# Performance work log

Hardware: AMD Instinct MI355X
Metric: run time of the kernel (lower is better)

The kernel has to match this reference:

```python
import jax, jax.numpy as jnp
from jax import lax
import numpy as np

B, GRID, H = 128, 28, 64      # batch, 28x28 pixel grid, hidden size
NDIR = 4                      # feature_sz = number of scan directions
FC_HD, OUT = 512, 10


def setup_inputs() -> dict:
    key = jax.random.key(0)
    ks = jax.random.split(key, 8)
    s_u = 1.0 / np.sqrt(2 * H)
    inp = {
        "x":  jax.random.normal(ks[0], (B, GRID, GRID), dtype=jnp.float32),
        # per-direction MDLSTM gate params: 5 gates (i, f_left, f_up, o, g)
        "Wx": jax.random.normal(ks[1], (NDIR, 5 * H), dtype=jnp.float32) * 0.1,
        "U":  jax.random.normal(ks[2], (NDIR, 2 * H, 5 * H), dtype=jnp.float32) * s_u,
        "b":  jnp.zeros((NDIR, 5 * H), dtype=jnp.float32),
        # fc head
        "W1": jax.random.normal(ks[3], (NDIR * H, FC_HD), dtype=jnp.float32) / np.sqrt(NDIR * H),
        "b1": jnp.zeros((FC_HD,), dtype=jnp.float32),
        "W2": jax.random.normal(ks[4], (FC_HD, OUT), dtype=jnp.float32) / np.sqrt(FC_HD),
        "b2": jnp.zeros((OUT,), dtype=jnp.float32),
    }
    return inp


def _mdlstm_dir(xg, Wx, U, b):
    # xg: [GRID(rows), GRID(cols), B] scalar pixel per cell
    zeros = jnp.zeros((xg.shape[-1], H), dtype=xg.dtype)

    def col_step(carry, inp):
        h_left, c_left = carry
        x_pix, h_up, c_up = inp                     # [B], [B,H], [B,H]
        z = x_pix[:, None] * Wx + jnp.concatenate([h_left, h_up], -1) @ U + b
        i, f1, f2, o, g = jnp.split(z, 5, axis=-1)  # each [B,H]
        c = (jax.nn.sigmoid(i) * jnp.tanh(g)
             + jax.nn.sigmoid(f1) * c_left
             + jax.nn.sigmoid(f2) * c_up)
        h = jax.nn.sigmoid(o) * jnp.tanh(c)
        return (h, c), (h, c)

    def row_step(carry, x_row):
        h_up_row, c_up_row = carry                  # [GRID,B,H] previous row
        _, (h_row, c_row) = lax.scan(col_step, (zeros, zeros),
                                     (x_row, h_up_row, c_up_row))
        return (h_row, c_row), None

    init = (jnp.zeros((GRID,) + zeros.shape, xg.dtype),
            jnp.zeros((GRID,) + zeros.shape, xg.dtype))
    (h_last_row, _), _ = lax.scan(row_step, init, xg)
    return h_last_row[-1]                           # final (bottom-right) hidden [B,H]


def _forward(x, Wx, U, b, W1, b1, W2, b2):
    x2 = x.reshape(-1, GRID, GRID)
    # 4 scan directions via flips; scan always proceeds top-left -> bottom-right
    dirs = jnp.stack([x2,
                      x2[:, :, ::-1],
                      x2[:, ::-1, :],
                      x2[:, ::-1, ::-1]], 0)        # [4,B,GRID,GRID]
    dirs = jnp.transpose(dirs, (0, 2, 3, 1))        # [4,GRID,GRID,B]
    h = jax.vmap(_mdlstm_dir)(dirs, Wx, U, b)       # [4,B,H]
    h = jnp.transpose(h, (1, 0, 2)).reshape(-1, NDIR * H)
    z = jax.nn.relu(h @ W1 + b1)
    return jax.nn.softmax(z @ W2 + b2, axis=-1)


def reference(x, Wx, U, b, W1, b1, W2, b2):
    return _forward(x, Wx, U, b, W1, b1, W2, b2)
```

## Files before the change

kernel.cpp:

```cpp
#include <hip/hip_runtime.h>
#include <hip/hip_bf16.h>


#define GRIDN 28
#define BATCH 128
#define HID   64
#define NDIR  4
#define FC_HD 512
#define OUT_N 10
#define BT    2
#define NTHR  512
#define NSLOT 29
#define S_H   104
#define S_C   68

typedef _Float16 f16;
typedef _Float16 f16x8 __attribute__((ext_vector_type(8)));
typedef float    f32x4 __attribute__((ext_vector_type(4)));

#define LOG2E  1.44269504088896340736f
#define LOG2E2 2.88539008177792681472f

__device__ __forceinline__ float rcpf(float x) { return __builtin_amdgcn_rcpf(x); }
__device__ __forceinline__ float ex2(float x)  { return __builtin_amdgcn_exp2f(x); }

__global__ __launch_bounds__(NTHR)
void mdlstm_kernel(const float* __restrict__ x,
                   const float* __restrict__ Wx,
                   const float* __restrict__ U,
                   const float* __restrict__ bias,
                   float* __restrict__ Hout)
{
    const int d    = blockIdx.x & 3;
    const int tile = blockIdx.x >> 2;
    const int tid  = threadIdx.x;
    const int lane = tid & 63;
    const int wave = tid >> 6;
    const int wm   = wave >> 2;
    const int wh   = wave & 3;
    const int l16  = lane & 15;
    const int q    = lane >> 4;
    const int nb   = wh * 16 + l16;

    __shared__ __align__(16) f16 Fh[2][BT][NSLOT * S_H];
    __shared__ float             Fc[2][BT][NSLOT * S_C];
    __shared__ float             xs[GRIDN][GRIDN][BT];

    for (int i = tid; i < 2 * BT * NSLOT * S_H; i += NTHR) ((f16*)Fh)[i] = (f16)0.0f;
    for (int i = tid; i < 2 * BT * NSLOT * S_C; i += NTHR) ((float*)Fc)[i] = 0.0f;
    for (int i = tid; i < GRIDN * GRIDN * BT; i += NTHR) {
        int bl = i & 1, rc = i >> 1, c = rc % GRIDN, r = rc / GRIDN;
        int rr = (d & 2) ? (GRIDN - 1 - r) : r;
        int cc = (d & 1) ? (GRIDN - 1 - c) : c;
        xs[r][c][bl] = x[((tile * BT + bl) * GRIDN + rr) * GRIDN + cc];
    }

    f16x8 bf[5][5];
#pragma unroll
    for (int g = 0; g < 5; ++g) {
        const float sc = (g == 4) ? LOG2E2 : -LOG2E;
        int n = g * 64 + nb;
#pragma unroll
        for (int ks = 0; ks < 4; ++ks) {
            f16x8 v;
            int kb = ks * 32 + q * 8;
#pragma unroll
            for (int j = 0; j < 8; ++j)
                v[j] = (f16)(sc * U[(d * 128 + kb + j) * 320 + n]);
            bf[g][ks] = v;
        }
        f16x8 v5 = {(f16)0, (f16)0, (f16)0, (f16)0, (f16)0, (f16)0, (f16)0, (f16)0};
        if (q == 0) {
            v5[0] = (f16)(sc * Wx[d * 320 + n]);
            v5[1] = (f16)(sc * bias[d * 320 + n]);
        }
        bf[g][4] = v5;
    }
    __syncthreads();

    if (tid < 2 * BT * NSLOT) {
        int buf = tid / (BT * NSLOT), rem = tid % (BT * NSLOT);
        int b = rem / NSLOT, sl = rem % NSLOT;
        Fh[buf][b][sl * S_H + 65] = (f16)1.0f;
    }
    if (tid < BT) Fh[0][tid][27 * S_H + 64] = (f16)xs[0][0][tid];
    __syncthreads();

    auto step = [&](int t, int br) __attribute__((always_inline)) {
        const int bw  = br ^ 1;
        const int rlo = (t > GRIDN - 1) ? (t - (GRIDN - 1)) : 0;
        const int rhi = (t < GRIDN - 1) ? t : (GRIDN - 1);
        const int k   = rhi - rlo + 1;
        const int nM  = (2 * k + 15) >> 4;

        if (t < 2 * GRIDN - 2 && tid >= NTHR - 56) {
            int idx = tid - (NTHR - 56), b = idx & 1, j = idx >> 1;
            int rlo2 = (t + 1 > GRIDN - 1) ? (t + 1 - (GRIDN - 1)) : 0;
            int rhi2 = (t + 1 < GRIDN - 1) ? (t + 1) : (GRIDN - 1);
            if (j <= rhi2 - rlo2) {
                int r = rlo2 + j;
                Fh[bw][b][(27 - r) * S_H + 64] = (f16)xs[r][t + 1 - r][b];
            }
        }

        for (int mt = wm; mt < nM; mt += 2) {
            int mA = mt * 16 + l16;
            int jA = mA >> 1; if (jA > k - 1) jA = k - 1;
            int bA = mA & 1;
            int slA = 27 - (rlo + jA);
            const f16* ab = &Fh[br][bA][slA * S_H];
            f16x8 a0 = *(const f16x8*)(ab + q * 8);
            f16x8 a1 = *(const f16x8*)(ab + 32 + q * 8);
            f16x8 a2 = *(const f16x8*)(ab + S_H + q * 8);
            f16x8 a3 = *(const f16x8*)(ab + S_H + 32 + q * 8);
            f16x8 a4 = *(const f16x8*)(ab + 64 + q * 8);

            int j0  = mt * 8 + q * 2;
            int jj0 = (j0     > k - 1) ? k - 1 : j0;
            int jj1 = (j0 + 1 > k - 1) ? k - 1 : j0 + 1;
            int sl0 = 27 - (rlo + jj0);
            int sl1 = 27 - (rlo + jj1);
            const float* rp[4] = { &Fc[br][0][sl0 * S_C + nb], &Fc[br][1][sl0 * S_C + nb],
                                   &Fc[br][0][sl1 * S_C + nb], &Fc[br][1][sl1 * S_C + nb] };
            float pcl[4], pcu[4];
#pragma unroll
            for (int i = 0; i < 4; ++i) { pcl[i] = rp[i][0]; pcu[i] = rp[i][S_C]; }

            const f32x4 z4 = {0.f, 0.f, 0.f, 0.f};
            f32x4 acc[5];
#pragma unroll
            for (int g = 0; g < 5; ++g) acc[g] = __builtin_amdgcn_mfma_f32_16x16x32_f16(a4, bf[g][4], z4, 0, 0, 0);
#pragma unroll
            for (int g = 0; g < 5; ++g) acc[g] = __builtin_amdgcn_mfma_f32_16x16x32_f16(a0, bf[g][0], acc[g], 0, 0, 0);
#pragma unroll
            for (int g = 0; g < 5; ++g) acc[g] = __builtin_amdgcn_mfma_f32_16x16x32_f16(a1, bf[g][1], acc[g], 0, 0, 0);
#pragma unroll
            for (int g = 0; g < 5; ++g) acc[g] = __builtin_amdgcn_mfma_f32_16x16x32_f16(a2, bf[g][2], acc[g], 0, 0, 0);
#pragma unroll
            for (int g = 0; g < 5; ++g) acc[g] = __builtin_amdgcn_mfma_f32_16x16x32_f16(a3, bf[g][3], acc[g], 0, 0, 0);

            const int DC = (bw - br) * (BT * NSLOT * S_C);
            int ih0 = sl0 * S_H + nb, ih1 = sl1 * S_H + nb;
            f16* wh0 = &Fh[bw][0][0];
            f16* wh1 = &Fh[bw][1][0];
#pragma unroll
            for (int i = 0; i < 4; ++i) {
                float ta = 1.0f + ex2(acc[0][i]);
                float tp = 1.0f + ex2(acc[1][i]);
                float tq = 1.0f + ex2(acc[2][i]);
                float td = 1.0f + ex2(acc[3][i]);
                float tb = 1.0f + ex2(acc[4][i]);
                float cn = (tb - 2.0f) * rcpf(ta * tb)
                         + (pcl[i] * tq + pcu[i] * tp) * rcpf(tp * tq);
                float cnc = fminf(cn, 22.0f);
                float te = 1.0f + ex2(LOG2E2 * cnc);
                float hn = (te - 2.0f) * rcpf(td * te);
                *(float*)(rp[i] + DC) = cn;
                ((i & 1) ? wh1 : wh0)[(i < 2) ? ih0 : ih1] = (f16)hn;
            }
        }
        __syncthreads();
    };

    for (int tb = 0; tb < 27; ++tb) { step(2 * tb, 0); step(2 * tb + 1, 1); }
    step(54, 0);

    if (tid < BT * HID) {
        int bl = tid >> 6, h = tid & 63;
        Hout[(d * BATCH + tile * BT + bl) * HID + h] = (float)Fh[1][bl][h];
    }
}

__global__ __launch_bounds__(256)
void fc_kernel(const float* __restrict__ Hin,
               const float* __restrict__ W1, const float* __restrict__ b1,
               const float* __restrict__ W2, const float* __restrict__ b2,
               float* __restrict__ out)
{
    const int b   = blockIdx.x;
    const int tid = threadIdx.x;
    __shared__ float hrow[NDIR * HID];
    __shared__ float z1[FC_HD];
    __shared__ float ps[16][16];
    __shared__ float z2[16];

    hrow[tid] = Hin[(tid >> 6) * (BATCH * HID) + b * HID + (tid & 63)];
    __syncthreads();

    {
        float s0 = b1[tid], s1 = b1[tid + 256];
#pragma unroll 8
        for (int f = 0; f < NDIR * HID; ++f) {
            float h = hrow[f];
            s0 += h * W1[f * FC_HD + tid];
            s1 += h * W1[f * FC_HD + tid + 256];
        }
        z1[tid]       = fmaxf(s0, 0.0f);
        z1[tid + 256] = fmaxf(s1, 0.0f);
    }
    __syncthreads();

    {
        int j = tid & 15, sl = tid >> 4;
        float s = 0.0f;
        if (j < OUT_N) {
#pragma unroll
            for (int i = 0; i < 32; ++i) {
                int kk = sl * 32 + i;
                s += z1[kk] * W2[kk * OUT_N + j];
            }
        }
        ps[sl][j] = s;
    }
    __syncthreads();

    if (tid < OUT_N) {
        float s = b2[tid];
#pragma unroll
        for (int sl = 0; sl < 16; ++sl) s += ps[sl][tid];
        z2[tid] = s;
    }
    __syncthreads();

    if (tid == 0) {
        float m = z2[0];
        for (int j = 1; j < OUT_N; ++j) m = fmaxf(m, z2[j]);
        float sum = 0.0f, e[OUT_N];
        for (int j = 0; j < OUT_N; ++j) { e[j] = __expf(z2[j] - m); sum += e[j]; }
        float inv = 1.0f / sum;
        for (int j = 0; j < OUT_N; ++j) out[b * OUT_N + j] = e[j] * inv;
    }
}

extern "C" void kernel_launch(void* const* d_in, const int* in_sizes, int n_in,
                              void* d_out, int out_size, void* d_ws, size_t ws_size,
                              hipStream_t stream) {
    const float* x  = (const float*)d_in[0];
    const float* Wx = (const float*)d_in[1];
    const float* U  = (const float*)d_in[2];
    const float* bs = (const float*)d_in[3];
    const float* W1 = (const float*)d_in[4];
    const float* b1 = (const float*)d_in[5];
    const float* W2 = (const float*)d_in[6];
    const float* b2 = (const float*)d_in[7];
    float* out = (float*)d_out;
    float* Hws = (float*)d_ws;

    mdlstm_kernel<<<NDIR * (BATCH / BT), NTHR, 0, stream>>>(x, Wx, U, bs, Hws);
    fc_kernel<<<BATCH, 256, 0, stream>>>(Hws, W1, b1, W2, b2, out);
}
```

Measured before the change: 152.2 us.

## Assign fixed rows per wave, keep left cell state in registers

New measurement: 168.0 us. +10.3%, slower.

```diff
diff --git a/kernel.cpp b/kernel.cpp
--- a/kernel.cpp
+++ b/kernel.cpp
@@ -44,18 +44,12 @@
 
     __shared__ __align__(16) f16 Fh[2][BT][NSLOT * S_H];
     __shared__ float             Fc[2][BT][NSLOT * S_C];
-    __shared__ float             xs[GRIDN][GRIDN][BT];
 
     for (int i = tid; i < 2 * BT * NSLOT * S_H; i += NTHR) ((f16*)Fh)[i] = (f16)0.0f;
     for (int i = tid; i < 2 * BT * NSLOT * S_C; i += NTHR) ((float*)Fc)[i] = 0.0f;
-    for (int i = tid; i < GRIDN * GRIDN * BT; i += NTHR) {
-        int bl = i & 1, rc = i >> 1, c = rc % GRIDN, r = rc / GRIDN;
-        int rr = (d & 2) ? (GRIDN - 1 - r) : r;
-        int cc = (d & 1) ? (GRIDN - 1 - c) : c;
-        xs[r][c][bl] = x[((tile * BT + bl) * GRIDN + rr) * GRIDN + cc];
-    }
-
-    f16x8 bf[5][5];
+
+    f16x8 bf[5][4];
+    float sWx[5], sB[5];
 #pragma unroll
     for (int g = 0; g < 5; ++g) {
         const float sc = (g == 4) ? LOG2E2 : -LOG2E;
@@ -69,96 +63,124 @@
                 v[j] = (f16)(sc * U[(d * 128 + kb + j) * 320 + n]);
             bf[g][ks] = v;
         }
-        f16x8 v5 = {(f16)0, (f16)0, (f16)0, (f16)0, (f16)0, (f16)0, (f16)0, (f16)0};
-        if (q == 0) {
-            v5[0] = (f16)(sc * Wx[d * 320 + n]);
-            v5[1] = (f16)(sc * bias[d * 320 + n]);
-        }
-        bf[g][4] = v5;
-    }
-    __syncthreads();
-
-    if (tid < 2 * BT * NSLOT) {
-        int buf = tid / (BT * NSLOT), rem = tid % (BT * NSLOT);
-        int b = rem / NSLOT, sl = rem % NSLOT;
-        Fh[buf][b][sl * S_H + 65] = (f16)1.0f;
-    }
-    if (tid < BT) Fh[0][tid][27 * S_H + 64] = (f16)xs[0][0][tid];
-    __syncthreads();
-
-    auto step = [&](int t, int br) __attribute__((always_inline)) {
-        const int bw  = br ^ 1;
-        const int rlo = (t > GRIDN - 1) ? (t - (GRIDN - 1)) : 0;
-        const int rhi = (t < GRIDN - 1) ? t : (GRIDN - 1);
-        const int k   = rhi - rlo + 1;
-        const int nM  = (2 * k + 15) >> 4;
-
-        if (t < 2 * GRIDN - 2 && tid >= NTHR - 56) {
-            int idx = tid - (NTHR - 56), b = idx & 1, j = idx >> 1;
-            int rlo2 = (t + 1 > GRIDN - 1) ? (t + 1 - (GRIDN - 1)) : 0;
-            int rhi2 = (t + 1 < GRIDN - 1) ? (t + 1) : (GRIDN - 1);
-            if (j <= rhi2 - rlo2) {
-                int r = rlo2 + j;
-                Fh[bw][b][(27 - r) * S_H + 64] = (f16)xs[r][t + 1 - r][b];
-            }
-        }
-
-        for (int mt = wm; mt < nM; mt += 2) {
-            int mA = mt * 16 + l16;
-            int jA = mA >> 1; if (jA > k - 1) jA = k - 1;
-            int bA = mA & 1;
-            int slA = 27 - (rlo + jA);
-            const f16* ab = &Fh[br][bA][slA * S_H];
-            f16x8 a0 = *(const f16x8*)(ab + q * 8);
-            f16x8 a1 = *(const f16x8*)(ab + 32 + q * 8);
-            f16x8 a2 = *(const f16x8*)(ab + S_H + q * 8);
-            f16x8 a3 = *(const f16x8*)(ab + S_H + 32 + q * 8);
-            f16x8 a4 = *(const f16x8*)(ab + 64 + q * 8);
-
-            int j0  = mt * 8 + q * 2;
-            int jj0 = (j0     > k - 1) ? k - 1 : j0;
-            int jj1 = (j0 + 1 > k - 1) ? k - 1 : j0 + 1;
-            int sl0 = 27 - (rlo + jj0);
-            int sl1 = 27 - (rlo + jj1);
-            const float* rp[4] = { &Fc[br][0][sl0 * S_C + nb], &Fc[br][1][sl0 * S_C + nb],
-                                   &Fc[br][0][sl1 * S_C + nb], &Fc[br][1][sl1 * S_C + nb] };
-            float pcl[4], pcu[4];
-#pragma unroll
-            for (int i = 0; i < 4; ++i) { pcl[i] = rp[i][0]; pcu[i] = rp[i][S_C]; }
-
-            const f32x4 z4 = {0.f, 0.f, 0.f, 0.f};
-            f32x4 acc[5];
-#pragma unroll
-            for (int g = 0; g < 5; ++g) acc[g] = __builtin_amdgcn_mfma_f32_16x16x32_f16(a4, bf[g][4], z4, 0, 0, 0);
-#pragma unroll
-            for (int g = 0; g < 5; ++g) acc[g] = __builtin_amdgcn_mfma_f32_16x16x32_f16(a0, bf[g][0], acc[g], 0, 0, 0);
-#pragma unroll
-            for (int g = 0; g < 5; ++g) acc[g] = __builtin_amdgcn_mfma_f32_16x16x32_f16(a1, bf[g][1], acc[g], 0, 0, 0);
-#pragma unroll
-            for (int g = 0; g < 5; ++g) acc[g] = __builtin_amdgcn_mfma_f32_16x16x32_f16(a2, bf[g][2], acc[g], 0, 0, 0);
-#pragma unroll
-            for (int g = 0; g < 5; ++g) acc[g] = __builtin_amdgcn_mfma_f32_16x16x32_f16(a3, bf[g][3], acc[g], 0, 0, 0);
-
-            const int DC = (bw - br) * (BT * NSLOT * S_C);
-            int ih0 = sl0 * S_H + nb, ih1 = sl1 * S_H + nb;
-            f16* wh0 = &Fh[bw][0][0];
-            f16* wh1 = &Fh[bw][1][0];
+        sWx[g] = sc * Wx[d * 320 + n];
+        sB[g]  = sc * bias[d * 320 + n];
+    }
+
+    int aoffs[2];
+#pragma unroll
+    for (int u = 0; u < 2; ++u) {
+        int mA = (wm + 2 * u) * 16 + l16;
+        int rA = mA >> 1; if (rA > GRIDN - 1) rA = GRIDN - 1;
+        int bA = mA & 1;
+        aoffs[u] = (bA * NSLOT + (27 - rA)) * S_H + q * 8;
+    }
+    int rw[2][4], hoffs[2][4], coffs[2][4], xoffs[2][4];
+#pragma unroll
+    for (int u = 0; u < 2; ++u)
+#pragma unroll
+        for (int i = 0; i < 4; ++i) {
+            int mrow = (wm + 2 * u) * 16 + q * 4 + i;
+            int r = mrow >> 1; if (r > GRIDN - 1) r = GRIDN - 1;
+            int b = mrow & 1;
+            rw[u][i]    = r;
+            hoffs[u][i] = (b * NSLOT + (27 - r)) * S_H + nb;
+            coffs[u][i] = (b * NSLOT + (27 - r)) * S_C + nb;
+            int rr = (d & 2) ? (GRIDN - 1 - r) : r;
+            xoffs[u][i] = ((tile * BT + b) * GRIDN + rr) * GRIDN;
+        }
+
+    float creg[2][4] = {{0.f,0.f,0.f,0.f},{0.f,0.f,0.f,0.f}};
+
+    __syncthreads();
+
+    auto tasks = [&](int t, const f16* FhR, f16* FhW,
+                     const float* FcR, float* FcW,
+                     int ulo, int ucnt) __attribute__((always_inline)) {
+        f16x8 a[2][4];
+        float xv[2][4], pcu[2][4];
+        bool  act[2][4];
+#pragma unroll
+        for (int k = 0; k < ucnt; ++k) {
+            const int u = ulo + k;
+            const f16* ab = FhR + aoffs[u];
+            a[u][0] = *(const f16x8*)(ab);
+            a[u][1] = *(const f16x8*)(ab + 32);
+            a[u][2] = *(const f16x8*)(ab + S_H);
+            a[u][3] = *(const f16x8*)(ab + S_H + 32);
+        }
+#pragma unroll
+        for (int k = 0; k < ucnt; ++k) {
+            const int u = ulo + k;
 #pragma unroll
             for (int i = 0; i < 4; ++i) {
-                float ta = 1.0f + ex2(acc[0][i]);
-                float tp = 1.0f + ex2(acc[1][i]);
-                float tq = 1.0f + ex2(acc[2][i]);
-                float td = 1.0f + ex2(acc[3][i]);
-                float tb = 1.0f + ex2(acc[4][i]);
+                int r = rw[u][i];
+                int c = t - r;
+                act[u][i] = ((unsigned)c <= 27u);
+                c = c < 0 ? 0 : (c > 27 ? 27 : c);
+                int cc = (d & 1) ? (GRIDN - 1 - c) : c;
+                xv[u][i]  = x[xoffs[u][i] + cc];
+                pcu[u][i] = FcR[coffs[u][i] + S_C];
+            }
+        }
+        f32x4 acc[2][5];
+#pragma unroll
+        for (int k = 0; k < ucnt; ++k) {
+            const int u = ulo + k;
+#pragma unroll
+            for (int g = 0; g < 5; ++g) {
+                f32x4 ci;
+#pragma unroll
+                for (int i = 0; i < 4; ++i) ci[i] = sB[g] + sWx[g] * xv[u][i];
+                acc[u][g] = ci;
+            }
+        }
+#pragma unroll
+        for (int ks = 0; ks < 4; ++ks)
+#pragma unroll
+            for (int k = 0; k < ucnt; ++k) {
+                const int u = ulo + k;
+#pragma unroll
+                for (int g = 0; g < 5; ++g)
+                    acc[u][g] = __builtin_amdgcn_mfma_f32_16x16x32_f16(
+                        a[u][ks], bf[g][ks], acc[u][g], 0, 0, 0);
+            }
+#pragma unroll
+        for (int k = 0; k < ucnt; ++k) {
+            const int u = ulo + k;
+#pragma unroll
+            for (int i = 0; i < 4; ++i) {
+                float ta = 1.0f + ex2(acc[u][0][i]);
+                float tp = 1.0f + ex2(acc[u][1][i]);
+                float tq = 1.0f + ex2(acc[u][2][i]);
+                float td = 1.0f + ex2(acc[u][3][i]);
+                float tb = 1.0f + ex2(acc[u][4][i]);
                 float cn = (tb - 2.0f) * rcpf(ta * tb)
-                         + (pcl[i] * tq + pcu[i] * tp) * rcpf(tp * tq);
+                         + (creg[u][i] * tq + pcu[u][i] * tp) * rcpf(tp * tq);
                 float cnc = fminf(cn, 22.0f);
                 float te = 1.0f + ex2(LOG2E2 * cnc);
                 float hn = (te - 2.0f) * rcpf(td * te);
-                *(float*)(rp[i] + DC) = cn;
-                ((i & 1) ? wh1 : wh0)[(i < 2) ? ih0 : ih1] = (f16)hn;
-            }
-        }
+                if (act[u][i]) {
+                    creg[u][i] = cn;
+                    FcW[coffs[u][i]] = cn;
+                    FhW[hoffs[u][i]] = (f16)hn;
+                }
+            }
+        }
+    };
+
+    auto step = [&](int t, int br) __attribute__((always_inline)) {
+        const int bw = br ^ 1;
+        const f16*   FhR = &Fh[br][0][0];
+        f16*         FhW = &Fh[bw][0][0];
+        const float* FcR = &Fc[br][0][0];
+        float*       FcW = &Fc[bw][0][0];
+        const int T0 = wm, T1 = wm + 2;
+        bool a0v = (8 * T0 <= t) && (t <= 8 * T0 + 34);
+        bool a1v = (8 * T1 <= t) && (t <= 8 * T1 + 34);
+        if (a0v && a1v)      tasks(t, FhR, FhW, FcR, FcW, 0, 2);
+        else if (a0v)        tasks(t, FhR, FhW, FcR, FcW, 0, 1);
+        else if (a1v)        tasks(t, FhR, FhW, FcR, FcW, 1, 1);
         __syncthreads();
     };
 
```

## Fuse FC head into MDLSTM kernel using per-tile completion flags

Applied to the files above, without the earlier changes.

Result: slower. 188.9 us (+24.1%).

```diff
diff --git a/kernel.cpp b/kernel.cpp
--- a/kernel.cpp
+++ b/kernel.cpp
@@ -29,7 +29,13 @@
                    const float* __restrict__ Wx,
                    const float* __restrict__ U,
                    const float* __restrict__ bias,
-                   float* __restrict__ Hout)
+                   float* __restrict__ Hout,
+                   const float* __restrict__ W1,
+                   const float* __restrict__ fb1,
+                   const float* __restrict__ W2,
+                   const float* __restrict__ fb2,
+                   float* __restrict__ out,
+                   unsigned* __restrict__ flags)
 {
     const int d    = blockIdx.x & 3;
     const int tile = blockIdx.x >> 2;
@@ -45,6 +51,14 @@
     __shared__ __align__(16) f16 Fh[2][BT][NSLOT * S_H];
     __shared__ float             Fc[2][BT][NSLOT * S_C];
     __shared__ float             xs[GRIDN][GRIDN][BT];
+    __shared__ float hrow2[BT][NDIR * HID];
+    __shared__ float z1s[BT][FC_HD];
+    __shared__ float ps2[BT][16][16];
+    __shared__ float z2s[BT][16];
+
+    if (flags && d < 3 && tid == 0)
+        __hip_atomic_store(&flags[tile * 4 + d], 0u,
+                           __ATOMIC_RELAXED, __HIP_MEMORY_SCOPE_AGENT);
 
     for (int i = tid; i < 2 * BT * NSLOT * S_H; i += NTHR) ((f16*)Fh)[i] = (f16)0.0f;
     for (int i = tid; i < 2 * BT * NSLOT * S_C; i += NTHR) ((float*)Fc)[i] = 0.0f;
@@ -169,6 +183,79 @@
         int bl = tid >> 6, h = tid & 63;
         Hout[(d * BATCH + tile * BT + bl) * HID + h] = (float)Fh[1][bl][h];
     }
+
+    if (!flags) return;
+    __syncthreads();
+
+    if (d < 3) {
+        if (tid == 0) {
+            __threadfence();
+            __hip_atomic_store(&flags[tile * 4 + d],
+                               0x5EEDBE00u | (unsigned)(tile * 4 + d),
+                               __ATOMIC_RELEASE, __HIP_MEMORY_SCOPE_AGENT);
+        }
+        return;
+    }
+
+    if (tid < 3) {
+        unsigned want = 0x5EEDBE00u | (unsigned)(tile * 4 + tid);
+        while (__hip_atomic_load(&flags[tile * 4 + tid],
+                                 __ATOMIC_ACQUIRE, __HIP_MEMORY_SCOPE_AGENT) != want)
+            __builtin_amdgcn_s_sleep(2);
+    }
+    __syncthreads();
+    __threadfence();
+
+    const int g = tid >> 8;
+    const int t = tid & 255;
+    const int b = tile * BT + g;
+
+    hrow2[g][t] = Hout[(t >> 6) * (BATCH * HID) + b * HID + (t & 63)];
+    __syncthreads();
+
+    {
+        float s0 = fb1[t], s1 = fb1[t + 256];
+#pragma unroll 8
+        for (int f = 0; f < NDIR * HID; ++f) {
+            float h = hrow2[g][f];
+            s0 += h * W1[f * FC_HD + t];
+            s1 += h * W1[f * FC_HD + t + 256];
+        }
+        z1s[g][t]       = fmaxf(s0, 0.0f);
+        z1s[g][t + 256] = fmaxf(s1, 0.0f);
+    }
+    __syncthreads();
+
+    {
+        int j = t & 15, sl = t >> 4;
+        float s = 0.0f;
+        if (j < OUT_N) {
+#pragma unroll
+            for (int i = 0; i < 32; ++i) {
+                int kk = sl * 32 + i;
+                s += z1s[g][kk] * W2[kk * OUT_N + j];
+            }
+        }
+        ps2[g][sl][j] = s;
+    }
+    __syncthreads();
+
+    if (t < OUT_N) {
+        float s = fb2[t];
+#pragma unroll
+        for (int sl = 0; sl < 16; ++sl) s += ps2[g][sl][t];
+        z2s[g][t] = s;
+    }
+    __syncthreads();
+
+    if (t == 0) {
+        float m = z2s[g][0];
+        for (int j = 1; j < OUT_N; ++j) m = fmaxf(m, z2s[g][j]);
+        float sum = 0.0f, e[OUT_N];
+        for (int j = 0; j < OUT_N; ++j) { e[j] = __expf(z2s[g][j] - m); sum += e[j]; }
+        float inv = 1.0f / sum;
+        for (int j = 0; j < OUT_N; ++j) out[b * OUT_N + j] = e[j] * inv;
+    }
 }
 
 __global__ __launch_bounds__(256)
@@ -246,6 +333,12 @@
     float* out = (float*)d_out;
     float* Hws = (float*)d_ws;
 
-    mdlstm_kernel<<<NDIR * (BATCH / BT), NTHR, 0, stream>>>(x, Wx, U, bs, Hws);
-    fc_kernel<<<BATCH, 256, 0, stream>>>(Hws, W1, b1, W2, b2, out);
+    const size_t hbytes = (size_t)NDIR * BATCH * HID * sizeof(float);
+    bool fused = ws_size >= hbytes + 256 * sizeof(unsigned);
+    unsigned* flags = fused ? (unsigned*)((char*)d_ws + hbytes) : nullptr;
+
+    mdlstm_kernel<<<NDIR * (BATCH / BT), NTHR, 0, stream>>>(
+        x, Wx, U, bs, Hws, W1, b1, W2, b2, out, flags);
+    if (!fused)
+        fc_kernel<<<BATCH, 256, 0, stream>>>(Hws, W1, b1, W2, b2, out);
 }
```
